# Kernel tuning notes

Hardware: AMD Instinct MI355X
Metric: run time of the kernel (lower is better)

The kernel has to match this reference:

```python
import jax, jax.numpy as jnp
import numpy as np

B, T, S1, S2 = 8, 64, 128, 128
TD, SD, V, PAD = 512, 512, 32000, 0
EXT = V + S1 + S2
EPS = 1e-5


def _ln(x):
    # F.layer_norm with no affine params (biased variance, eps=1e-5)
    m = x.mean(axis=-1, keepdims=True)
    v = ((x - m) ** 2).mean(axis=-1, keepdims=True)
    return (x - m) / jnp.sqrt(v + EPS)


def _cross_attention(q, k, q_mask, k_mask, attn_w, attn_b, v_vec):
    # attn(cat(q,k)) == q @ Wq^T + k @ Wk^T + b, computed without materializing the concat
    Wq = attn_w[:, :TD]          # [TD, TD] (query part of weight: cat order is (query, key))
    Wk = attn_w[:, TD:]          # [TD, SD]
    sq = jnp.einsum('btd,ed->bte', q, Wq)   # [B,T,TD]
    sk = jnp.einsum('bsd,ed->bse', k, Wk)   # [B,S,TD]
    energy = jnp.tanh(sq[:, :, None, :] + sk[:, None, :, :] + attn_b)  # [B,T,S,TD]
    scores = jnp.einsum('btse,e->bts', energy, v_vec)                  # [B,T,S]
    out_att = scores * k_mask[:, None, :] * q_mask[:, :, None]
    masked = jnp.where((k_mask == PAD)[:, None, :], -jnp.inf, scores)
    attn = jax.nn.softmax(masked, axis=-1)
    weight = jnp.einsum('bts,bsd->btd', attn, k) * q_mask[:, :, None]  # [B,T,SD]
    return out_att, weight


def _scatter_copy(att, map_idx):
    # index_put_(accumulate=True) into [B,T,EXT]
    copy = jnp.zeros((B, T, EXT), dtype=att.dtype)
    b_idx = jnp.arange(B)[:, None, None]
    t_idx = jnp.arange(T)[None, :, None]
    m_idx = map_idx[:, None, :]
    return copy.at[b_idx, t_idx, m_idx].add(att)


def setup_inputs() -> dict:
    key = jax.random.key(0)
    ks = jax.random.split(key, 14)
    sc = 0.02
    return {
        'tgt_dec_out': jax.random.normal(ks[0], (B, T, TD), jnp.float32),
        'src1_key': jax.random.normal(ks[1], (B, S1, SD), jnp.float32),
        'src2_key': jax.random.normal(ks[2], (B, S2, SD), jnp.float32),
        'src1_map_idx': jax.random.randint(ks[3], (B, S1), 0, EXT),
        'src2_map_idx': jax.random.randint(ks[4], (B, S2), 0, EXT),
        'out_fc_w': jax.random.normal(ks[5], (V, TD), jnp.float32) * sc,
        'out_fc_b': jnp.zeros((V,), jnp.float32),
        'attn1_w': jax.random.normal(ks[6], (TD, SD + TD), jnp.float32) * sc,
        'attn1_b': jnp.zeros((TD,), jnp.float32),
        'v1': jax.random.normal(ks[7], (TD,), jnp.float32) * sc,
        'attn2_w': jax.random.normal(ks[8], (TD, SD + TD), jnp.float32) * sc,
        'attn2_b': jnp.zeros((TD,), jnp.float32),
        'v2': jax.random.normal(ks[9], (TD,), jnp.float32) * sc,
        'gate_w': jax.random.normal(ks[10], (3, 2 * SD + TD), jnp.float32) * sc,
        'gate_b': jnp.zeros((3,), jnp.float32),
    }


def reference(tgt_dec_out, src1_key, src2_key, src1_map_idx, src2_map_idx,
              out_fc_w, out_fc_b, attn1_w, attn1_b, v1, attn2_w, attn2_b, v2,
              gate_w, gate_b):
    tgt_output = _ln(jnp.einsum('btd,vd->btv', tgt_dec_out, out_fc_w) + out_fc_b)
    tgt_output = jnp.pad(tgt_output, ((0, 0), (0, 0), (0, S1 + S2)), constant_values=float(PAD))

    tgt_mask = jnp.sign(jnp.abs(tgt_dec_out).sum(-1))   # [B,T]
    src1_mask = jnp.sign(jnp.abs(src1_key).sum(-1))     # [B,S1]
    src2_mask = jnp.sign(jnp.abs(src2_key).sum(-1))     # [B,S2]

    att1, c1 = _cross_attention(tgt_dec_out, src1_key, tgt_mask, src1_mask, attn1_w, attn1_b, v1)
    att1 = _ln(att1)
    copy_output1 = _scatter_copy(att1, src1_map_idx)

    att2, c2 = _cross_attention(tgt_dec_out, src2_key, tgt_mask, src2_mask, attn2_w, attn2_b, v2)
    att2 = _ln(att2)
    copy_output2 = _scatter_copy(att2, src2_map_idx)

    gate_in = jnp.concatenate([tgt_dec_out, c1, c2], axis=-1)  # [B,T,TD+2*SD]
    p = jax.nn.softmax(jnp.einsum('btd,pd->btp', gate_in, gate_w) + gate_b, axis=-1)  # [B,T,3]

    output = (tgt_output * p[..., 0:1]
              + copy_output1 * p[..., 1:2]
              + copy_output2 * p[..., 2:3])
    return output
```

## Files before the change

### kernel.cpp

```cpp
#include <hip/hip_runtime.h>

#define NB 8
#define NT 64
#define NS 128
#define TDIM 512
#define NV 32000
#define NEXT 32256
#define NBT 512
#define LNEPS 1e-5f
#define CLG 2.8853900817779268f

typedef unsigned short u16;
typedef __attribute__((ext_vector_type(8))) short short8;
typedef __attribute__((ext_vector_type(4))) float f32x4;

__device__ __forceinline__ float bf2f(u16 u){ union{unsigned int i; float f;} v; v.i = ((unsigned int)u)<<16; return v.f; }
__device__ __forceinline__ u16 f2bf(float f){ union{float f; unsigned int i;} v; v.f=f; unsigned int r = v.i + 0x7FFFu + ((v.i>>16)&1u); return (u16)(r>>16); }
__device__ __forceinline__ float wsum(float v){
  v += __shfl_xor(v,32); v += __shfl_xor(v,16); v += __shfl_xor(v,8);
  v += __shfl_xor(v,4);  v += __shfl_xor(v,2);  v += __shfl_xor(v,1); return v; }
__device__ __forceinline__ float wmax(float v){
  v = fmaxf(v,__shfl_xor(v,32)); v = fmaxf(v,__shfl_xor(v,16)); v = fmaxf(v,__shfl_xor(v,8));
  v = fmaxf(v,__shfl_xor(v,4));  v = fmaxf(v,__shfl_xor(v,2));  v = fmaxf(v,__shfl_xor(v,1)); return v; }

#define GL2LDS(gp, lp) __builtin_amdgcn_global_load_lds( \
    (__attribute__((address_space(1))) void*)(void*)(gp), \
    (__attribute__((address_space(3))) void*)(void*)(lp), 16, 0, 0)

__global__ __launch_bounds__(256) void k_cast(const float* tgt, const float* s1, const float* s2,
    const float* a1w, const float* a2w, const float* ofw,
    u16* tgtb, u16* s1b, u16* s2b, u16* a1wb, u16* a2wb, u16* ofwb, float* msk)
{
  int blk = blockIdx.x;
  const float* src; u16* dst; int base;
  if(blk < 128){       src=tgt; dst=tgtb;  base=blk; }
  else if(blk < 384){  src=s1;  dst=s1b;   base=blk-128; }
  else if(blk < 640){  src=s2;  dst=s2b;   base=blk-384; }
  else if(blk < 896){  src=a1w; dst=a1wb;  base=blk-640; }
  else if(blk < 1152){ src=a2w; dst=a2wb;  base=blk-896; }
  else {               src=ofw; dst=ofwb;  base=blk-1152; }
  size_t off = (size_t)base*2048 + (size_t)threadIdx.x*8;
  float4 x0 = *(const float4*)(src+off);
  float4 x1 = *(const float4*)(src+off+4);
  float xs[8] = {x0.x,x0.y,x0.z,x0.w,x1.x,x1.y,x1.z,x1.w};
  short8 r;
  #pragma unroll
  for(int j=0;j<8;++j) r[j] = (short)f2bf(xs[j]);
  *(short8*)(dst+off) = r;
  if(blk < 640){
    float a = 0.f;
    #pragma unroll
    for(int j=0;j<8;++j) a += fabsf(xs[j]);
    a = wsum(a);
    if((threadIdx.x&63)==0){
      int w = threadIdx.x>>6;
      int midx;
      if(blk<128)      midx = blk*4 + w;
      else if(blk<384) midx = 512 + (blk-128)*4 + w;
      else             midx = 1536 + (blk-384)*4 + w;
      msk[midx] = (a>0.f) ? 1.f : 0.f;
    }
  }
}

__device__ __forceinline__ void gemm_core2(u16* Al, u16* Wl, const u16* A, int lda, const u16* W, int ldw,
    float* Cf, int ldc, const float* bias, int K, int bm, int bn, float scale)
{
  const int tid = threadIdx.x, lane = tid&63, wv = tid>>6;
  const int wm = wv>>1, wn = wv&1;
  const int fr = lane&15, fq = lane>>4;
  const int lrow = lane>>2;
  const int lcol = (lane&3)*8;
  f32x4 acc[4][4] = {};
  for(int k0=0;k0<K;k0+=32){
    #pragma unroll
    for(int r=0;r<2;++r){
      int c = wv + 4*r;
      int row = c*16 + lrow;
      const u16* ga = A + (size_t)(bm+row)*lda + k0 + lcol;
      const u16* gw = W + (size_t)(bn+row)*ldw + k0 + lcol;
      GL2LDS(ga, &Al[c*512]);
      GL2LDS(gw, &Wl[c*512]);
    }
    __syncthreads();
    short8 af[4], bfr[4];
    #pragma unroll
    for(int m=0;m<4;++m) af[m] = *(const short8*)&Al[(wm*64 + m*16 + fr)*32 + fq*8];
    #pragma unroll
    for(int n=0;n<4;++n) bfr[n] = *(const short8*)&Wl[(wn*64 + n*16 + fr)*32 + fq*8];
    #pragma unroll
    for(int m=0;m<4;++m)
      #pragma unroll
      for(int n=0;n<4;++n)
        acc[m][n] = __builtin_amdgcn_mfma_f32_16x16x32_bf16(af[m], bfr[n], acc[m][n], 0,0,0);
    __syncthreads();
  }
  #pragma unroll
  for(int m=0;m<4;++m)
    #pragma unroll
    for(int n=0;n<4;++n)
      #pragma unroll
      for(int i=0;i<4;++i){
        int row = bm + wm*64 + m*16 + fq*4 + i;
        int col = bn + wn*64 + n*16 + fr;
        float bv = bias ? bias[col] : 0.f;
        Cf[(size_t)row*ldc + col] = (acc[m][n][i] + bv)*scale;
      }
}

__global__ __launch_bounds__(256) void k_bigproj(const u16* A, const u16* W, const float* bias,
    u16* logits, float2* pstats,
    const u16* s1, const u16* s2, const u16* w1, const u16* w2,
    const float* b1, const float* b2,
    float* sq1, float* sk1, float* sq2, float* sk2)
{
  __shared__ u16 Al[128*32];
  __shared__ u16 Wl[128*32];
  __shared__ float ps_s[2][64], pq_s[2][64];

  if(blockIdx.x >= 2000){
    int p = blockIdx.x - 2000;
    int z = p>>5, y = (p>>2)&7, x = p&3;
    int Mt = (z&1) ? 1024 : 512;
    int bm = y*128; if(bm >= Mt) return;
    const u16* Ap = (z&1) ? ((z>>1) ? s2 : s1) : A;
    const u16* Wp = ((z>>1) ? w2 : w1) + ((z&1) ? TDIM : 0);
    float* Cf = (z==0) ? sq1 : (z==1) ? sk1 : (z==2) ? sq2 : sk2;
    const float* bp = (z&1) ? nullptr : ((z>>1) ? b2 : b1);
    gemm_core2(Al, Wl, Ap, TDIM, Wp, 2*TDIM, Cf, TDIM, bp, TDIM, bm, x*128, CLG);
    return;
  }

  int lid = (blockIdx.x&7)*250 + (blockIdx.x>>3);
  int bm = (lid&7)*64, bn = (lid>>3)*128, nb = lid>>3;
  const int tid = threadIdx.x, lane = tid&63, wv = tid>>6;
  const int wm = wv>>1, wn = wv&1;
  const int fr = lane&15, fq = lane>>4;
  const int lrow = lane>>2;
  const int lcol = (lane&3)*8;
  f32x4 acc[2][4] = {};
  for(int k0=0;k0<512;k0+=32){
    GL2LDS(A + (size_t)(bm + wv*16 + lrow)*512 + k0 + lcol, &Wl[wv*512]);
    #pragma unroll
    for(int r=0;r<2;++r){
      int c = wv + 4*r;
      GL2LDS(W + (size_t)(bn + c*16 + lrow)*512 + k0 + lcol, &Al[c*512]);
    }
    __syncthreads();
    short8 af[2], bfr[4];
    #pragma unroll
    for(int m=0;m<2;++m) af[m] = *(const short8*)&Wl[(wm*32 + m*16 + fr)*32 + fq*8];
    #pragma unroll
    for(int n=0;n<4;++n) bfr[n] = *(const short8*)&Al[(wn*64 + n*16 + fr)*32 + fq*8];
    #pragma unroll
    for(int m=0;m<2;++m)
      #pragma unroll
      for(int n=0;n<4;++n)
        acc[m][n] = __builtin_amdgcn_mfma_f32_16x16x32_bf16(af[m], bfr[n], acc[m][n], 0,0,0);
    __syncthreads();
  }

  #pragma unroll
  for(int m=0;m<2;++m){
    float rs_[4]={0,0,0,0}, rq_[4]={0,0,0,0};
    #pragma unroll
    for(int n=0;n<4;++n)
      #pragma unroll
      for(int i=0;i<4;++i){
        int row = bm + wm*32 + m*16 + fq*4 + i;
        int col = bn + wn*64 + n*16 + fr;
        float v = acc[m][n][i] + bias[col];
        logits[(size_t)row*NV + col] = f2bf(v);
        rs_[i] += v; rq_[i] += v*v;
      }
    #pragma unroll
    for(int i=0;i<4;++i){
      float a=rs_[i], q=rq_[i];
      a+=__shfl_xor(a,1); a+=__shfl_xor(a,2); a+=__shfl_xor(a,4); a+=__shfl_xor(a,8);
      q+=__shfl_xor(q,1); q+=__shfl_xor(q,2); q+=__shfl_xor(q,4); q+=__shfl_xor(q,8);
      if(fr==0){ int lr = wm*32 + m*16 + fq*4 + i; ps_s[wn][lr]=a; pq_s[wn][lr]=q; }
    }
  }
  __syncthreads();
  if(tid<64){
    float2 pv;
    pv.x = ps_s[0][tid]+ps_s[1][tid];
    pv.y = pq_s[0][tid]+pq_s[1][tid];
    pstats[(size_t)(bm+tid)*250 + nb] = pv;
  }
}

__global__ __launch_bounds__(256) void k_energy(
  const float* sq1, const float* sq2, const float* sk1, const float* sk2,
  const float* v1p, const float* v2p, float* pene)
{
  int lid = (blockIdx.x&7)*128 + (blockIdx.x>>3);
  int src = lid>>9, b = (lid>>6)&7, tc = (lid>>4)&3, sc = (lid>>2)&3, eq = lid&3;
  int tid = threadIdx.x;
  const float* SQ = src? sq2:sq1;
  const float* SK = src? sk2:sk1;
  const float* vp = src? v2p:v1p;
  int t0 = tc*16, s0 = sc*32;
  int strow = tid&31, trow = tid>>5;

  __shared__ float sk_lds[32*65];
  float acc_a = 0.f, acc_b = 0.f;
  const float* sqa = SQ + (size_t)(b*64 + t0 + trow)*512;
  const float* sqb = sqa + 8*512;

  for(int ec=eq*2; ec<eq*2+2; ++ec){
    {
      int r = tid>>3, c0 = (tid&7)*8;
      const float* sp = SK + (size_t)(b*128 + s0 + r)*512 + ec*64 + c0;
      float4 A0 = *(const float4*)sp;
      float4 A1 = *(const float4*)(sp+4);
      float* dp = &sk_lds[r*65 + c0];
      dp[0]=A0.x; dp[1]=A0.y; dp[2]=A0.z; dp[3]=A0.w;
      dp[4]=A1.x; dp[5]=A1.y; dp[6]=A1.z; dp[7]=A1.w;
    }
    __syncthreads();
    #pragma unroll
    for(int sub=0; sub<4; ++sub){
      int e0 = ec*64 + sub*16;
      float4 V0 = *(const float4*)(vp+e0),    V1 = *(const float4*)(vp+e0+4);
      float4 V2 = *(const float4*)(vp+e0+8),  V3 = *(const float4*)(vp+e0+12);
      float4 QA0 = *(const float4*)(sqa+e0),  QA1 = *(const float4*)(sqa+e0+4);
      float4 QA2 = *(const float4*)(sqa+e0+8),QA3 = *(const float4*)(sqa+e0+12);
      float4 QB0 = *(const float4*)(sqb+e0),  QB1 = *(const float4*)(sqb+e0+4);
      float4 QB2 = *(const float4*)(sqb+e0+8),QB3 = *(const float4*)(sqb+e0+12);
      float vv[16] = {V0.x,V0.y,V0.z,V0.w,V1.x,V1.y,V1.z,V1.w,V2.x,V2.y,V2.z,V2.w,V3.x,V3.y,V3.z,V3.w};
      float qa[16] = {QA0.x,QA0.y,QA0.z,QA0.w,QA1.x,QA1.y,QA1.z,QA1.w,QA2.x,QA2.y,QA2.z,QA2.w,QA3.x,QA3.y,QA3.z,QA3.w};
      float qb[16] = {QB0.x,QB0.y,QB0.z,QB0.w,QB1.x,QB1.y,QB1.z,QB1.w,QB2.x,QB2.y,QB2.z,QB2.w,QB3.x,QB3.y,QB3.z,QB3.w};
      const float* skr = &sk_lds[strow*65 + sub*16];
      #pragma unroll
      for(int e=0;e<16;++e){
        float skv = skr[e];
        float ya = qa[e] + skv;
        float yb = qb[e] + skv;
        float ra = __builtin_amdgcn_rcpf(__builtin_amdgcn_exp2f(ya) + 1.f);
        float rb = __builtin_amdgcn_rcpf(__builtin_amdgcn_exp2f(yb) + 1.f);
        acc_a = __builtin_fmaf(vv[e], ra, acc_a);
        acc_b = __builtin_fmaf(vv[e], rb, acc_b);
      }
    }
    __syncthreads();
  }
  size_t ia = (size_t)((eq*2+src)*512 + b*64 + t0 + trow)*128 + s0 + strow;
  pene[ia] = acc_a;
  pene[ia + 8*128] = acc_b;
}

__global__ __launch_bounds__(256) void k_sm(
  const float* pene, const float* v1p, const float* v2p,
  const float* k1g, const float* k2g, const float* msk,
  float* al1, float* al2, float* c1, float* c2)
{
  int lid = (blockIdx.x&7)*32 + (blockIdx.x>>3);
  int src = lid>>7, b = (lid>>4)&7, tq = lid&15;
  int tid = threadIdx.x, lane = tid&63, wv = tid>>6;
  int t = tq*4 + wv, bt = b*64 + t;
  const float* vp = src? v2p:v1p;
  const float* kg = src? k2g:k1g;
  float* al = src? al2:al1;
  float* cc = src? c2:c1;
  const float* km_g = msk + 512 + src*1024 + b*128;
  __shared__ float aw_lds[4][132];
  __shared__ float qm_lds[4];

  {
    float vsp = 0.f;
    #pragma unroll
    for(int r2=0;r2<8;++r2) vsp += vp[lane + 64*r2];
    float Vsum = wsum(vsp);
    float qm = msk[bt];
    float km0 = km_g[lane], km1 = km_g[lane+64];
    size_t pbase = (size_t)(src*512 + bt)*128;
    float p0a = pene[pbase + lane]          + pene[pbase + 131072 + lane];
    float p0b = pene[pbase + 262144 + lane] + pene[pbase + 393216 + lane];
    float p1a = pene[pbase + lane + 64]          + pene[pbase + 131072 + lane + 64];
    float p1b = pene[pbase + 262144 + lane + 64] + pene[pbase + 393216 + lane + 64];
    float s0v = Vsum - 2.f*(p0a + p0b);
    float s1v = Vsum - 2.f*(p1a + p1b);
    float a0 = s0v*km0*qm, a1 = s1v*km1*qm;
    float sm = wsum(a0+a1), sqq = wsum(a0*a0+a1*a1);
    float m0 = km0!=0.f ? s0v : -1e30f;
    float m1 = km1!=0.f ? s1v : -1e30f;
    float mx = wmax(fmaxf(m0,m1));
    float e0 = km0!=0.f ? __expf(s0v-mx) : 0.f;
    float e1 = km1!=0.f ? __expf(s1v-mx) : 0.f;
    float den = wsum(e0+e1);
    float mean = sm/128.f;
    float inv  = rsqrtf(sqq/128.f - mean*mean + LNEPS);
    al[(size_t)bt*128 + lane]      = (a0-mean)*inv;
    al[(size_t)bt*128 + lane + 64] = (a1-mean)*inv;
    float rden = 1.f/den;
    aw_lds[wv][lane]      = e0*rden;
    aw_lds[wv][lane+64]   = e1*rden;
    if(lane==0) qm_lds[wv] = qm;
  }
  __syncthreads();
  {
    float acc[4][2] = {};
    const float* kb = kg + (size_t)b*128*512;
    for(int s=0;s<128;++s){
      float kv0 = kb[(size_t)s*512 + tid];
      float kv1 = kb[(size_t)s*512 + tid + 256];
      #pragma unroll
      for(int w=0;w<4;++w){
        float a = aw_lds[w][s];
        acc[w][0] = __builtin_fmaf(a, kv0, acc[w][0]);
        acc[w][1] = __builtin_fmaf(a, kv1, acc[w][1]);
      }
    }
    #pragma unroll
    for(int w=0;w<4;++w){
      float qm = qm_lds[w];
      size_t o = (size_t)(b*64 + tq*4 + w)*512;
      cc[o + tid]       = qm*acc[w][0];
      cc[o + tid + 256] = qm*acc[w][1];
    }
  }
}

__global__ __launch_bounds__(256) void k_out(const u16* logits, const float2* pstats,
    const float* al1, const float* al2, const float* c1, const float* c2,
    const float* tgt, const float* gw, const float* gb,
    const int* map1, const int* map2, float* out)
{
  int row = blockIdx.x>>2, q = blockIdx.x&3, b = row>>6;
  int tid = threadIdx.x, lane = tid&63, wv = tid>>6;
  __shared__ float gred[4][3], rs[4], rq[4], st[2], pl_s[3];
  __shared__ int hkey[1024];
  __shared__ float hval[1024];
  __shared__ unsigned int bmap[252];

  #pragma unroll
  for(int r=0;r<4;++r){ hkey[tid+256*r] = -1; hval[tid+256*r] = 0.f; }
  if(tid < 252) bmap[tid] = 0u;

  {
    float t0v = tgt[(size_t)row*512+tid], t1v = tgt[(size_t)row*512+tid+256];
    float c10 = c1[(size_t)row*512+tid],  c11 = c1[(size_t)row*512+tid+256];
    float c20 = c2[(size_t)row*512+tid],  c21 = c2[(size_t)row*512+tid+256];
    #pragma unroll
    for(int p=0;p<3;++p){
      const float* gp = gw + p*1536;
      float a = gp[tid]*t0v + gp[tid+256]*t1v
              + gp[512+tid]*c10 + gp[768+tid]*c11
              + gp[1024+tid]*c20 + gp[1280+tid]*c21;
      a = wsum(a);
      if(lane==0) gred[wv][p] = a;
    }
  }
  {
    float s=0.f, qv=0.f;
    if(tid < 250){ float2 pv = pstats[(size_t)row*250 + tid]; s = pv.x; qv = pv.y; }
    s = wsum(s); qv = wsum(qv);
    if(lane==0){ rs[wv]=s; rq[wv]=qv; }
  }
  __syncthreads();
  if(tid==0){
    float S = rs[0]+rs[1]+rs[2]+rs[3];
    float Q = rq[0]+rq[1]+rq[2]+rq[3];
    float mean = S/(float)NV;
    float var  = Q/(float)NV - mean*mean;
    st[0] = mean; st[1] = rsqrtf(var+LNEPS);
    float g0 = gred[0][0]+gred[1][0]+gred[2][0]+gred[3][0] + gb[0];
    float g1 = gred[0][1]+gred[1][1]+gred[2][1]+gred[3][1] + gb[1];
    float g2 = gred[0][2]+gred[1][2]+gred[2][2]+gred[3][2] + gb[2];
    float m = fmaxf(g0, fmaxf(g1, g2));
    float e0=__expf(g0-m), e1=__expf(g1-m), e2=__expf(g2-m);
    float sI = 1.f/(e0+e1+e2);
    pl_s[0]=e0*sI; pl_s[1]=e1*sI; pl_s[2]=e2*sI;
  }
  __syncthreads();

  int elo = q*8064;
  {
    int src = tid>>7, sl = tid&127;
    int e = (src ? map2 : map1)[b*128 + sl];
    if(e >= elo && e < elo+8064){
      float val = pl_s[1+src] * (src ? al2 : al1)[(size_t)row*128 + sl];
      unsigned int h = ((unsigned int)e * 2654435761u) >> 22;
      for(;;){
        int old = atomicCAS(&hkey[h], -1, e);
        if(old == -1 || old == e){ atomicAdd(&hval[h], val); break; }
        h = (h+1) & 1023;
      }
      int rel = e - elo;
      atomicOr(&bmap[rel>>5], 1u << (rel&31));
    }
  }
  __syncthreads();

  float mean = st[0], inv = st[1], p0 = pl_s[0];
  const u16* Lr = logits + (size_t)row*NV;
  float* orow = out + (size_t)row*NEXT;
  for(int i=q*2016+tid; i<(q+1)*2016; i+=256){
    int e0 = i*4;
    float4 r;
    if(e0 < NV){
      const u16* L = &Lr[e0];
      r.x = p0*(bf2f(L[0])-mean)*inv;
      r.y = p0*(bf2f(L[1])-mean)*inv;
      r.z = p0*(bf2f(L[2])-mean)*inv;
      r.w = p0*(bf2f(L[3])-mean)*inv;
    } else { r.x=r.y=r.z=r.w=0.f; }
    int rel = e0 - elo;
    unsigned int w4 = (bmap[rel>>5] >> (rel&31)) & 0xFu;
    if(w4){
      #pragma unroll
      for(int j=0;j<4;++j){
        if(w4 & (1u<<j)){
          int e = e0 + j;
          unsigned int h = ((unsigned int)e * 2654435761u) >> 22;
          while(hkey[h] != e) h = (h+1) & 1023;
          float pv = hval[h];
          if(j==0) r.x += pv; else if(j==1) r.y += pv; else if(j==2) r.z += pv; else r.w += pv;
        }
      }
    }
    *(float4*)&orow[e0] = r;
  }
}

extern "C" void kernel_launch(void* const* d_in, const int* in_sizes, int n_in,
                              void* d_out, int out_size, void* d_ws, size_t ws_size,
                              hipStream_t stream)
{
  const float* tgt  = (const float*)d_in[0];
  const float* s1k  = (const float*)d_in[1];
  const float* s2k  = (const float*)d_in[2];
  const int*   map1 = (const int*)d_in[3];
  const int*   map2 = (const int*)d_in[4];
  const float* ofw  = (const float*)d_in[5];
  const float* ofb  = (const float*)d_in[6];
  const float* a1w  = (const float*)d_in[7];
  const float* a1b  = (const float*)d_in[8];
  const float* v1   = (const float*)d_in[9];
  const float* a2w  = (const float*)d_in[10];
  const float* a2b  = (const float*)d_in[11];
  const float* v2   = (const float*)d_in[12];
  const float* gw   = (const float*)d_in[13];
  const float* gb   = (const float*)d_in[14];

  float* wsf   = (float*)d_ws;
  float* sq1   = wsf;
  float* sq2   = wsf + 262144;
  float* sk1   = wsf + 524288;
  float* sk2   = wsf + 1048576;
  float* al1   = wsf + 1572864;
  float* al2   = wsf + 1638400;
  float* msk   = wsf + 1705984;
  float* c1    = wsf + 1709568;
  float* c2    = wsf + 1971712;
  float* pene  = wsf + 2233856;
  float2* pstats = (float2*)(wsf + 2758144);
  u16*  logits = (u16*)(wsf + 3014144);
  u16*  tgtb   = (u16*)(wsf + 11206144);
  u16*  s1b    = (u16*)(wsf + 11337216);
  u16*  s2b    = (u16*)(wsf + 11599360);
  u16*  a1wb   = (u16*)(wsf + 11861504);
  u16*  a2wb   = (u16*)(wsf + 12123648);
  u16*  ofwb   = (u16*)(wsf + 12385792);
  float* out   = (float*)d_out;

  k_cast   <<<9152, 256, 0, stream>>>(tgt, s1k, s2k, a1w, a2w, ofw, tgtb, s1b, s2b, a1wb, a2wb, ofwb, msk);
  k_bigproj<<<2128, 256, 0, stream>>>(tgtb, ofwb, ofb, logits, pstats,
                                      s1b, s2b, a1wb, a2wb, a1b, a2b, sq1, sk1, sq2, sk2);
  k_energy <<<1024, 256, 0, stream>>>(sq1, sq2, sk1, sk2, v1, v2, pene);
  k_sm     <<<256, 256, 0, stream>>>(pene, v1, v2, s1k, s2k, msk, al1, al2, c1, c2);
  k_out    <<<2048, 256, 0, stream>>>(logits, pstats, al1, al2, c1, c2, tgt, gw, gb, map1, map2, out);
}
```

Before: 114.5 us.

## Rebalance kernel stages: co-schedule out_fc cast with attention projections, big GEMM with energy

Reshuffles work across launches. The out_fc weight cast moves out of the first cast kernel into the projection kernel, so it runs alongside the small attention-projection GEMMs. The big vocabulary GEMM moves into the same launch as the tanh-energy computation, with their shared memory overlaid in a union. The aim is to overlap memory-bound and compute-bound work and cut the number of dependent launches, at the cost of more complex block dispatch and possible imbalance among blocks in the merged grids.

```diff
diff --git a/kernel.cpp b/kernel.cpp
--- a/kernel.cpp
+++ b/kernel.cpp
@@ -27,9 +27,9 @@
     (__attribute__((address_space(1))) void*)(void*)(gp), \
     (__attribute__((address_space(3))) void*)(void*)(lp), 16, 0, 0)
 
-__global__ __launch_bounds__(256) void k_cast(const float* tgt, const float* s1, const float* s2,
-    const float* a1w, const float* a2w, const float* ofw,
-    u16* tgtb, u16* s1b, u16* s2b, u16* a1wb, u16* a2wb, u16* ofwb, float* msk)
+__global__ __launch_bounds__(256) void k_cast_small(const float* tgt, const float* s1, const float* s2,
+    const float* a1w, const float* a2w,
+    u16* tgtb, u16* s1b, u16* s2b, u16* a1wb, u16* a2wb, float* msk)
 {
   int blk = blockIdx.x;
   const float* src; u16* dst; int base;
@@ -37,8 +37,7 @@
   else if(blk < 384){  src=s1;  dst=s1b;   base=blk-128; }
   else if(blk < 640){  src=s2;  dst=s2b;   base=blk-384; }
   else if(blk < 896){  src=a1w; dst=a1wb;  base=blk-640; }
-  else if(blk < 1152){ src=a2w; dst=a2wb;  base=blk-896; }
-  else {               src=ofw; dst=ofwb;  base=blk-1152; }
+  else {               src=a2w; dst=a2wb;  base=blk-896; }
   size_t off = (size_t)base*2048 + (size_t)threadIdx.x*8;
   float4 x0 = *(const float4*)(src+off);
   float4 x1 = *(const float4*)(src+off+4);
@@ -108,102 +107,116 @@
       }
 }
 
-__global__ __launch_bounds__(256) void k_bigproj(const u16* A, const u16* W, const float* bias,
-    u16* logits, float2* pstats,
-    const u16* s1, const u16* s2, const u16* w1, const u16* w2,
+__global__ __launch_bounds__(256) void k_projcast(
+    const u16* tgtb, const u16* s1, const u16* s2, const u16* w1, const u16* w2,
     const float* b1, const float* b2,
-    float* sq1, float* sk1, float* sq2, float* sk2)
+    float* sq1, float* sk1, float* sq2, float* sk2,
+    const float* ofw, u16* ofwb)
 {
   __shared__ u16 Al[128*32];
   __shared__ u16 Wl[128*32];
-  __shared__ float ps_s[2][64], pq_s[2][64];
-
-  if(blockIdx.x >= 2000){
-    int p = blockIdx.x - 2000;
+  if(blockIdx.x < 128){
+    int p = blockIdx.x;
     int z = p>>5, y = (p>>2)&7, x = p&3;
     int Mt = (z&1) ? 1024 : 512;
     int bm = y*128; if(bm >= Mt) return;
-    const u16* Ap = (z&1) ? ((z>>1) ? s2 : s1) : A;
+    const u16* Ap = (z&1) ? ((z>>1) ? s2 : s1) : tgtb;
     const u16* Wp = ((z>>1) ? w2 : w1) + ((z&1) ? TDIM : 0);
     float* Cf = (z==0) ? sq1 : (z==1) ? sk1 : (z==2) ? sq2 : sk2;
     const float* bp = (z&1) ? nullptr : ((z>>1) ? b2 : b1);
     gemm_core2(Al, Wl, Ap, TDIM, Wp, 2*TDIM, Cf, TDIM, bp, TDIM, bm, x*128, CLG);
     return;
   }
-
-  int lid = (blockIdx.x&7)*250 + (blockIdx.x>>3);
-  int bm = (lid&7)*64, bn = (lid>>3)*128, nb = lid>>3;
+  size_t off = (size_t)(blockIdx.x-128)*2048 + (size_t)threadIdx.x*8;
+  float4 x0 = *(const float4*)(ofw+off);
+  float4 x1 = *(const float4*)(ofw+off+4);
+  float xs[8] = {x0.x,x0.y,x0.z,x0.w,x1.x,x1.y,x1.z,x1.w};
+  short8 r;
+  #pragma unroll
+  for(int j=0;j<8;++j) r[j] = (short)f2bf(xs[j]);
+  *(short8*)(ofwb+off) = r;
+}
+
+__global__ __launch_bounds__(256) void k_bigen(const u16* A, const u16* W, const float* bias,
+    u16* logits, float2* pstats,
+    const float* sq1, const float* sq2, const float* sk1, const float* sk2,
+    const float* v1p, const float* v2p, float* pene)
+{
+  union __align__(16) SMem {
+    struct { u16 Wt[128*32]; u16 At[64*32]; float ps[2][64]; float pq[2][64]; } big;
+    float sk[32*65];
+  };
+  __shared__ SMem smem;
   const int tid = threadIdx.x, lane = tid&63, wv = tid>>6;
-  const int wm = wv>>1, wn = wv&1;
-  const int fr = lane&15, fq = lane>>4;
-  const int lrow = lane>>2;
-  const int lcol = (lane&3)*8;
-  f32x4 acc[2][4] = {};
-  for(int k0=0;k0<512;k0+=32){
-    GL2LDS(A + (size_t)(bm + wv*16 + lrow)*512 + k0 + lcol, &Wl[wv*512]);
-    #pragma unroll
-    for(int r=0;r<2;++r){
-      int c = wv + 4*r;
-      GL2LDS(W + (size_t)(bn + c*16 + lrow)*512 + k0 + lcol, &Al[c*512]);
+
+  if(blockIdx.x < 2000){
+    int lid = (blockIdx.x&7)*250 + (blockIdx.x>>3);
+    int bm = (lid&7)*64, bn = (lid>>3)*128, nb = lid>>3;
+    const int wm = wv>>1, wn = wv&1;
+    const int fr = lane&15, fq = lane>>4;
+    const int lrow = lane>>2;
+    const int lcol = (lane&3)*8;
+    f32x4 acc[2][4] = {};
+    for(int k0=0;k0<512;k0+=32){
+      GL2LDS(A + (size_t)(bm + wv*16 + lrow)*512 + k0 + lcol, &smem.big.At[wv*512]);
+      #pragma unroll
+      for(int r=0;r<2;++r){
+        int c = wv + 4*r;
+        GL2LDS(W + (size_t)(bn + c*16 + lrow)*512 + k0 + lcol, &smem.big.Wt[c*512]);
+      }
+      __syncthreads();
+      short8 af[2], bfr[4];
+      #pragma unroll
+      for(int m=0;m<2;++m) af[m] = *(const short8*)&smem.big.At[(wm*32 + m*16 + fr)*32 + fq*8];
+      #pragma unroll
+      for(int n=0;n<4;++n) bfr[n] = *(const short8*)&smem.big.Wt[(wn*64 + n*16 + fr)*32 + fq*8];
+      #pragma unroll
+      for(int m=0;m<2;++m)
+        #pragma unroll
+        for(int n=0;n<4;++n)
+          acc[m][n] = __builtin_amdgcn_mfma_f32_16x16x32_bf16(af[m], bfr[n], acc[m][n], 0,0,0);
+      __syncthreads();
+    }
+    #pragma unroll
+    for(int m=0;m<2;++m){
+      float rs_[4]={0,0,0,0}, rq_[4]={0,0,0,0};
+      #pragma unroll
+      for(int n=0;n<4;++n)
+        #pragma unroll
+        for(int i=0;i<4;++i){
+          int row = bm + wm*32 + m*16 + fq*4 + i;
+          int col = bn + wn*64 + n*16 + fr;
+          float v = acc[m][n][i] + bias[col];
+          logits[(size_t)row*NV + col] = f2bf(v);
+          rs_[i] += v; rq_[i] += v*v;
+        }
+      #pragma unroll
+      for(int i=0;i<4;++i){
+        float a=rs_[i], q=rq_[i];
+        a+=__shfl_xor(a,1); a+=__shfl_xor(a,2); a+=__shfl_xor(a,4); a+=__shfl_xor(a,8);
+        q+=__shfl_xor(q,1); q+=__shfl_xor(q,2); q+=__shfl_xor(q,4); q+=__shfl_xor(q,8);
+        if(fr==0){ int lr = wm*32 + m*16 + fq*4 + i; smem.big.ps[wn][lr]=a; smem.big.pq[wn][lr]=q; }
+      }
     }
     __syncthreads();
-    short8 af[2], bfr[4];
-    #pragma unroll
-    for(int m=0;m<2;++m) af[m] = *(const short8*)&Wl[(wm*32 + m*16 + fr)*32 + fq*8];
-    #pragma unroll
-    for(int n=0;n<4;++n) bfr[n] = *(const short8*)&Al[(wn*64 + n*16 + fr)*32 + fq*8];
-    #pragma unroll
-    for(int m=0;m<2;++m)
-      #pragma unroll
-      for(int n=0;n<4;++n)
-        acc[m][n] = __builtin_amdgcn_mfma_f32_16x16x32_bf16(af[m], bfr[n], acc[m][n], 0,0,0);
-    __syncthreads();
-  }
-
-  #pragma unroll
-  for(int m=0;m<2;++m){
-    float rs_[4]={0,0,0,0}, rq_[4]={0,0,0,0};
-    #pragma unroll
-    for(int n=0;n<4;++n)
-      #pragma unroll
-      for(int i=0;i<4;++i){
-        int row = bm + wm*32 + m*16 + fq*4 + i;
-        int col = bn + wn*64 + n*16 + fr;
-        float v = acc[m][n][i] + bias[col];
-        logits[(size_t)row*NV + col] = f2bf(v);
-        rs_[i] += v; rq_[i] += v*v;
-      }
-    #pragma unroll
-    for(int i=0;i<4;++i){
-      float a=rs_[i], q=rq_[i];
-      a+=__shfl_xor(a,1); a+=__shfl_xor(a,2); a+=__shfl_xor(a,4); a+=__shfl_xor(a,8);
-      q+=__shfl_xor(q,1); q+=__shfl_xor(q,2); q+=__shfl_xor(q,4); q+=__shfl_xor(q,8);
-      if(fr==0){ int lr = wm*32 + m*16 + fq*4 + i; ps_s[wn][lr]=a; pq_s[wn][lr]=q; }
-    }
-  }
-  __syncthreads();
-  if(tid<64){
-    float2 pv;
-    pv.x = ps_s[0][tid]+ps_s[1][tid];
-    pv.y = pq_s[0][tid]+pq_s[1][tid];
-    pstats[(size_t)(bm+tid)*250 + nb] = pv;
-  }
-}
-
-__global__ __launch_bounds__(256) void k_energy(
-  const float* sq1, const float* sq2, const float* sk1, const float* sk2,
-  const float* v1p, const float* v2p, float* pene)
-{
-  int lid = (blockIdx.x&7)*128 + (blockIdx.x>>3);
+    if(tid<64){
+      float2 pv;
+      pv.x = smem.big.ps[0][tid]+smem.big.ps[1][tid];
+      pv.y = smem.big.pq[0][tid]+smem.big.pq[1][tid];
+      pstats[(size_t)(bm+tid)*250 + nb] = pv;
+    }
+    return;
+  }
+
+  int id = blockIdx.x - 2000;
+  int lid = (id&7)*128 + (id>>3);
   int src = lid>>9, b = (lid>>6)&7, tc = (lid>>4)&3, sc = (lid>>2)&3, eq = lid&3;
-  int tid = threadIdx.x;
   const float* SQ = src? sq2:sq1;
   const float* SK = src? sk2:sk1;
   const float* vp = src? v2p:v1p;
   int t0 = tc*16, s0 = sc*32;
   int strow = tid&31, trow = tid>>5;
 
-  __shared__ float sk_lds[32*65];
   float acc_a = 0.f, acc_b = 0.f;
   const float* sqa = SQ + (size_t)(b*64 + t0 + trow)*512;
   const float* sqb = sqa + 8*512;
@@ -214,7 +227,7 @@
       const float* sp = SK + (size_t)(b*128 + s0 + r)*512 + ec*64 + c0;
       float4 A0 = *(const float4*)sp;
       float4 A1 = *(const float4*)(sp+4);
-      float* dp = &sk_lds[r*65 + c0];
+      float* dp = &smem.sk[r*65 + c0];
       dp[0]=A0.x; dp[1]=A0.y; dp[2]=A0.z; dp[3]=A0.w;
       dp[4]=A1.x; dp[5]=A1.y; dp[6]=A1.z; dp[7]=A1.w;
     }
@@ -231,7 +244,7 @@
       float vv[16] = {V0.x,V0.y,V0.z,V0.w,V1.x,V1.y,V1.z,V1.w,V2.x,V2.y,V2.z,V2.w,V3.x,V3.y,V3.z,V3.w};
       float qa[16] = {QA0.x,QA0.y,QA0.z,QA0.w,QA1.x,QA1.y,QA1.z,QA1.w,QA2.x,QA2.y,QA2.z,QA2.w,QA3.x,QA3.y,QA3.z,QA3.w};
       float qb[16] = {QB0.x,QB0.y,QB0.z,QB0.w,QB1.x,QB1.y,QB1.z,QB1.w,QB2.x,QB2.y,QB2.z,QB2.w,QB3.x,QB3.y,QB3.z,QB3.w};
-      const float* skr = &sk_lds[strow*65 + sub*16];
+      const float* skr = &smem.sk[strow*65 + sub*16];
       #pragma unroll
       for(int e=0;e<16;++e){
         float skv = skr[e];
@@ -465,10 +478,11 @@
   u16*  ofwb   = (u16*)(wsf + 12385792);
   float* out   = (float*)d_out;
 
-  k_cast   <<<9152, 256, 0, stream>>>(tgt, s1k, s2k, a1w, a2w, ofw, tgtb, s1b, s2b, a1wb, a2wb, ofwb, msk);
-  k_bigproj<<<2128, 256, 0, stream>>>(tgtb, ofwb, ofb, logits, pstats,
-                                      s1b, s2b, a1wb, a2wb, a1b, a2b, sq1, sk1, sq2, sk2);
-  k_energy <<<1024, 256, 0, stream>>>(sq1, sq2, sk1, sk2, v1, v2, pene);
-  k_sm     <<<256, 256, 0, stream>>>(pene, v1, v2, s1k, s2k, msk, al1, al2, c1, c2);
-  k_out    <<<2048, 256, 0, stream>>>(logits, pstats, al1, al2, c1, c2, tgt, gw, gb, map1, map2, out);
-}
+  k_cast_small<<<1152, 256, 0, stream>>>(tgt, s1k, s2k, a1w, a2w, tgtb, s1b, s2b, a1wb, a2wb, msk);
+  k_projcast  <<<8128, 256, 0, stream>>>(tgtb, s1b, s2b, a1wb, a2wb, a1b, a2b,
+                                         sq1, sk1, sq2, sk2, ofw, ofwb);
+  k_bigen     <<<3024, 256, 0, stream>>>(tgtb, ofwb, ofb, logits, pstats,
+                                         sq1, sq2, sk1, sk2, v1, v2, pene);
+  k_sm        <<<256, 256, 0, stream>>>(pene, v1, v2, s1k, s2k, msk, al1, al2, c1, c2);
+  k_out       <<<2048, 256, 0, stream>>>(logits, pstats, al1, al2, c1, c2, tgt, gw, gb, map1, map2, out);
+}
```

After: 114.3 us. About the same (-0.1%).
